# Kernel tuning notes

Measured on AMD Instinct MI355X. Metric: run time of the kernel, lower is better.

Reference implementation:

```python
import jax, jax.numpy as jnp
import numpy as np

B = 2097152
CXR, ECG, EHR = 15, 14, 13
TOTAL = CXR + ECG + EHR  # 42
LN_EPS = 1e-5


def setup_inputs() -> dict:
    key = jax.random.key(0)
    ks = jax.random.split(key, 40)
    f32 = jnp.float32
    inp = {
        "cxr_probs": jax.random.normal(ks[0], (B, CXR), dtype=f32),
        "ecg_probs": jax.random.normal(ks[1], (B, ECG), dtype=f32),
        "ehr_probs": jax.random.normal(ks[2], (B, EHR), dtype=f32),
    }
    for i, (name, E) in enumerate([("cxr", CXR), ("ecg", ECG), ("ehr", EHR)]):
        k0 = 3 + i * 8
        s_in = 1.0 / np.sqrt(E)
        s_kv = 1.0 / np.sqrt(TOTAL)
        inp[f"in_w_{name}"] = jax.random.normal(ks[k0], (3 * E, E), dtype=f32) * s_in
        inp[f"in_b_{name}"] = jnp.zeros((3 * E,), dtype=f32)
        inp[f"out_w_{name}"] = jax.random.normal(ks[k0 + 1], (E, E), dtype=f32) * s_in
        inp[f"out_b_{name}"] = jnp.zeros((E,), dtype=f32)
        inp[f"kv_w_{name}"] = jax.random.normal(ks[k0 + 2], (E, TOTAL), dtype=f32) * s_kv
        inp[f"kv_b_{name}"] = jax.random.normal(ks[k0 + 3], (E,), dtype=f32) * s_kv
        inp[f"ln_g_{name}"] = jnp.ones((E,), dtype=f32)
        inp[f"ln_b_{name}"] = jnp.zeros((E,), dtype=f32)
    return inp


def _branch(x, ctx, in_w, in_b, out_w, out_b, kv_w, kv_b, ln_g, ln_b):
    # x: [B, E], ctx: [B, 42]
    E = x.shape[-1]
    kv = ctx @ kv_w.T + kv_b                      # [B, E]
    # nn.MultiheadAttention with q_len = kv_len = 1: softmax over a single
    # key is identically 1, so attn_out == v_proj(kv) exactly.
    Wv, bv = in_w[2 * E:], in_b[2 * E:]
    v = kv @ Wv.T + bv                            # [B, E]
    attended = v @ out_w.T + out_b                # [B, E]
    y = x + attended
    mu = jnp.mean(y, axis=-1, keepdims=True)
    var = jnp.mean(jnp.square(y - mu), axis=-1, keepdims=True)
    return (y - mu) * jax.lax.rsqrt(var + LN_EPS) * ln_g + ln_b


def reference(cxr_probs, ecg_probs, ehr_probs,
              in_w_cxr, in_b_cxr, out_w_cxr, out_b_cxr, kv_w_cxr, kv_b_cxr, ln_g_cxr, ln_b_cxr,
              in_w_ecg, in_b_ecg, out_w_ecg, out_b_ecg, kv_w_ecg, kv_b_ecg, ln_g_ecg, ln_b_ecg,
              in_w_ehr, in_b_ehr, out_w_ehr, out_b_ehr, kv_w_ehr, kv_b_ehr, ln_g_ehr, ln_b_ehr):
    ctx = jnp.concatenate([cxr_probs, ecg_probs, ehr_probs], axis=1)  # [B, 42]
    cxr_out = _branch(cxr_probs, ctx, in_w_cxr, in_b_cxr, out_w_cxr, out_b_cxr,
                      kv_w_cxr, kv_b_cxr, ln_g_cxr, ln_b_cxr)
    ecg_out = _branch(ecg_probs, ctx, in_w_ecg, in_b_ecg, out_w_ecg, out_b_ecg,
                      kv_w_ecg, kv_b_ecg, ln_g_ecg, ln_b_ecg)
    ehr_out = _branch(ehr_probs, ctx, in_w_ehr, in_b_ehr, out_w_ehr, out_b_ehr,
                      kv_w_ehr, kv_b_ehr, ln_g_ehr, ln_b_ehr)
    return (cxr_out, ecg_out, ehr_out)
```

## Files before the change

kernel.cpp:

```cpp
#include <hip/hip_runtime.h>
#include <stdint.h>

constexpr int CXR = 15, ECG = 14, EHR = 13;
constexpr int TOTAL = 42;
constexpr int MPITCH = 44;
constexpr float LN_EPS = 1e-5f;

constexpr int WS_M    = 0;
constexpr int WS_B    = TOTAL * MPITCH;
constexpr int WS_G    = WS_B + TOTAL;
constexpr int WS_BETA = WS_G + TOTAL;
constexpr int WS_FRAG = 1976;

constexpr int WROWS = 64;
constexpr int S0F = 0, S1F = WROWS * CXR, S2F = S1F + WROWS * ECG;
constexpr int SEG_F   = S2F + WROWS * EHR;
constexpr int ARENA_F = SEG_F + 8;
constexpr int WC0 = WROWS * CXR / 4, WC1 = WROWS * ECG / 4, WC2 = WROWS * EHR / 4;

typedef _Float16 half8 __attribute__((ext_vector_type(8)));
typedef float float4v __attribute__((ext_vector_type(4)));

struct FuseArgs {
    const float *in_w, *in_b, *out_w, *out_b, *kv_w, *kv_b, *ln_g, *ln_b;
    int E, R;
};

__global__ void fuse_weights_kernel(FuseArgs a0, FuseArgs a1, FuseArgs a2,
                                    float* __restrict__ ws) {
    FuseArgs a = (blockIdx.x == 0) ? a0 : (blockIdx.x == 1 ? a1 : a2);
    const int E = a.E, R = a.R;
    const int tid = threadIdx.x;

    __shared__ float T1[15 * 42];
    __shared__ float b1[15];

    for (int idx = tid; idx < E * TOTAL; idx += blockDim.x) {
        int i = idx / TOTAL, j = idx % TOTAL;
        float acc = 0.f;
        for (int k = 0; k < E; ++k)
            acc = fmaf(a.in_w[(2 * E + i) * E + k], a.kv_w[k * TOTAL + j], acc);
        T1[i * TOTAL + j] = acc;
    }
    if (tid < E) {
        float acc = a.in_b[2 * E + tid];
        for (int k = 0; k < E; ++k)
            acc = fmaf(a.in_w[(2 * E + tid) * E + k], a.kv_b[k], acc);
        b1[tid] = acc;
    }
    __syncthreads();

    for (int idx = tid; idx < E * MPITCH; idx += blockDim.x) {
        int i = idx / MPITCH, j = idx % MPITCH;
        float acc = 0.f;
        if (j < TOTAL)
            for (int k = 0; k < E; ++k)
                acc = fmaf(a.out_w[i * E + k], T1[k * TOTAL + j], acc);
        ws[WS_M + (R + i) * MPITCH + j] = acc;
    }
    if (tid < E) {
        float acc = a.out_b[tid];
        for (int k = 0; k < E; ++k)
            acc = fmaf(a.out_w[tid * E + k], b1[k], acc);
        ws[WS_B + R + tid]    = acc;
        ws[WS_G + R + tid]    = a.ln_g[tid];
        ws[WS_BETA + R + tid] = a.ln_b[tid];
    }
}

__global__ void fuse_frags_kernel(float* __restrict__ ws) {
    const int tid = threadIdx.x;
    if (tid >= 384) return;
    const int l = tid & 63, nt = tid >> 6;
    const int m = nt >> 1, t = nt & 1;
    const int j = l & 15;
    const int k0 = t * 32 + 8 * (l >> 4);
    const int offm = (m == 0) ? 0 : (m == 1 ? CXR : CXR + ECG);
    const int Em   = (m == 0) ? CXR : (m == 1 ? ECG : EHR);
    half8 h;
#pragma unroll
    for (int i = 0; i < 8; ++i) {
        int pos = k0 + i;
        int g = -1;
        if (pos < 15) g = pos;
        else if (pos >= 16 && pos < 30) g = pos - 1;
        else if (pos >= 32 && pos < 45) g = pos - 3;
        float v = 0.f;
        if (j < Em && g >= 0) {
            int gr = offm + j;
            v = ws[WS_M + gr * MPITCH + g];
            if (g == gr) v += 1.f;
        }
        h[i] = (_Float16)v;
    }
    ((half8*)(ws + WS_FRAG))[nt * 64 + l] = h;
}

template <int CH>
__device__ __forceinline__ void stage_seg(const float* __restrict__ g,
                                          float* lds_seg_base, int lane) {
#pragma unroll
    for (int it = 0; it < (CH + 63) / 64; ++it) {
        int idx = lane + it * 64;
        if (idx < CH) {
            const __attribute__((address_space(1))) void* src =
                (const __attribute__((address_space(1))) void*)
                    ((const char*)g + (size_t)idx * 16);
            __attribute__((address_space(3))) void* dst =
                (__attribute__((address_space(3))) void*)
                    ((char*)lds_seg_base + it * 1024);
            __builtin_amdgcn_global_load_lds(src, dst, 16, 0, 0);
        }
    }
}

__global__ __launch_bounds__(128, 4) void cmca_main(
        const float* __restrict__ cxr, const float* __restrict__ ecg,
        const float* __restrict__ ehr, const float* __restrict__ ws,
        float* __restrict__ out_cxr, float* __restrict__ out_ecg,
        float* __restrict__ out_ehr) {
    __shared__ __align__(16) float sbuf[2 * ARENA_F];
    const int tid = threadIdx.x;
    const int w = tid >> 6, lane = tid & 63;
    float* stg = sbuf + w * ARENA_F;
    const size_t gw = (size_t)blockIdx.x * 2 + w;
    const int h = lane >> 4, b15 = lane & 15;

    stage_seg<WC0>(cxr + gw * (size_t)(WROWS * CXR), stg + S0F, lane);
    stage_seg<WC1>(ecg + gw * (size_t)(WROWS * ECG), stg + S1F, lane);
    stage_seg<WC2>(ehr + gw * (size_t)(WROWS * EHR), stg + S2F, lane);

    const half8* fr = (const half8*)(ws + WS_FRAG);
    half8 wf[3][2];
#pragma unroll
    for (int m = 0; m < 3; ++m)
#pragma unroll
        for (int t = 0; t < 2; ++t) wf[m][t] = fr[(m * 2 + t) * 64 + lane];

    asm volatile("s_waitcnt vmcnt(0)" ::: "memory");
    __builtin_amdgcn_sched_barrier(0);

    const int e0    = (h < 2) ? 15 : 14;
    const int base0 = ((h < 2) ? S0F : S1F) + (h & 1) * 8;
    const int off1  = (h == 1) ? 8 : 0;

    float4v acc[3][4];
#pragma unroll
    for (int m = 0; m < 3; ++m)
#pragma unroll
        for (int n = 0; n < 4; ++n) acc[m][n] = float4v{0.f, 0.f, 0.f, 0.f};

#pragma unroll
    for (int n = 0; n < 4; ++n) {
        const int batch = n * 16 + b15;
        const float* p0 = stg + base0 + batch * e0;
        const float* p1 = stg + S2F + off1 + batch * 13;
        half8 x0, x1;
#pragma unroll
        for (int e = 0; e < 8; ++e) x0[e] = (_Float16)p0[e];
#pragma unroll
        for (int e = 0; e < 8; ++e) x1[e] = (_Float16)p1[e];
#pragma unroll
        for (int m = 0; m < 3; ++m) {
            acc[m][n] = __builtin_amdgcn_mfma_f32_16x16x32_f16(
                wf[m][0], x0, acc[m][n], 0, 0, 0);
            acc[m][n] = __builtin_amdgcn_mfma_f32_16x16x32_f16(
                wf[m][1], x1, acc[m][n], 0, 0, 0);
        }
    }

    constexpr int Earr[3] = {CXR, ECG, EHR};
    constexpr int OFFa[3] = {0, CXR, CXR + ECG};
    constexpr int SEGF[3] = {S0F, S1F, S2F};
#pragma unroll
    for (int m = 0; m < 3; ++m) {
        const int E = Earr[m];
        const float invE = 1.0f / E;
        float bs[4], gm[4], bt[4];
#pragma unroll
        for (int r = 0; r < 4; ++r) {
            int j = 4 * h + r;
            bool v = j < E;
            bs[r] = v ? ws[WS_B + OFFa[m] + j] : 0.f;
            gm[r] = v ? ws[WS_G + OFFa[m] + j] : 0.f;
            bt[r] = v ? ws[WS_BETA + OFFa[m] + j] : 0.f;
        }
#pragma unroll
        for (int n = 0; n < 4; ++n) {
            float y0 = acc[m][n][0] + bs[0];
            float y1 = acc[m][n][1] + bs[1];
            float y2 = acc[m][n][2] + bs[2];
            float y3 = acc[m][n][3] + bs[3];
            float s  = (y0 + y1) + (y2 + y3);
            float ss = y0 * y0;
            ss = fmaf(y1, y1, ss);
            ss = fmaf(y2, y2, ss);
            ss = fmaf(y3, y3, ss);
            s  += __shfl_xor(s, 16, 64);
            ss += __shfl_xor(ss, 16, 64);
            s  += __shfl_xor(s, 32, 64);
            ss += __shfl_xor(ss, 32, 64);
            float mu  = s * invE;
            float var = fmaf(ss, invE, -mu * mu);
            float rs  = rsqrtf(var + LN_EPS);
            const int row = n * 16 + b15;
            float yv[4] = {y0, y1, y2, y3};
#pragma unroll
            for (int r = 0; r < 4; ++r) {
                int j = 4 * h + r;
                if (j < E)
                    stg[SEGF[m] + row * E + j] =
                        fmaf((yv[r] - mu) * rs, gm[r], bt[r]);
            }
        }
    }

    const float4v* w4 = (const float4v*)stg;
    float4v* o0 = (float4v*)(out_cxr + gw * (size_t)(WROWS * CXR));
    float4v* o1 = (float4v*)(out_ecg + gw * (size_t)(WROWS * ECG));
    float4v* o2 = (float4v*)(out_ehr + gw * (size_t)(WROWS * EHR));
#pragma unroll
    for (int it = 0; it < 4; ++it) {
        int idx = lane + it * 64;
        if (idx < WC0) o0[idx] = w4[idx];
    }
#pragma unroll
    for (int it = 0; it < 4; ++it) {
        int idx = lane + it * 64;
        if (idx < WC1) o1[idx] = w4[WC0 + idx];
    }
#pragma unroll
    for (int it = 0; it < 4; ++it) {
        int idx = lane + it * 64;
        if (idx < WC2) o2[idx] = w4[WC0 + WC1 + idx];
    }
}

extern "C" void kernel_launch(void* const* d_in, const int* in_sizes, int n_in,
                              void* d_out, int out_size, void* d_ws, size_t ws_size,
                              hipStream_t stream) {
    const float* cxr = (const float*)d_in[0];
    const float* ecg = (const float*)d_in[1];
    const float* ehr = (const float*)d_in[2];
    float* ws = (float*)d_ws;
    float* out = (float*)d_out;

    const size_t Bn = (size_t)in_sizes[0] / CXR;

    auto mk = [&](int base, int E, int R) {
        FuseArgs a;
        a.in_w  = (const float*)d_in[base + 0];
        a.in_b  = (const float*)d_in[base + 1];
        a.out_w = (const float*)d_in[base + 2];
        a.out_b = (const float*)d_in[base + 3];
        a.kv_w  = (const float*)d_in[base + 4];
        a.kv_b  = (const float*)d_in[base + 5];
        a.ln_g  = (const float*)d_in[base + 6];
        a.ln_b  = (const float*)d_in[base + 7];
        a.E = E; a.R = R;
        return a;
    };
    FuseArgs a0 = mk(3, CXR, 0);
    FuseArgs a1 = mk(11, ECG, CXR);
    FuseArgs a2 = mk(19, EHR, CXR + ECG);

    fuse_weights_kernel<<<3, 256, 0, stream>>>(a0, a1, a2, ws);
    fuse_frags_kernel<<<1, 384, 0, stream>>>(ws);

    const int nblocks = (int)(Bn / (WROWS * 2));
    cmca_main<<<nblocks, 128, 0, stream>>>(cxr, ecg, ehr, ws,
                                           out,
                                           out + Bn * CXR,
                                           out + Bn * (CXR + ECG));
}
```

Baseline: 152.2 us.

## Repack staged inputs into swizzled fp16 rows with bias folded into GEMM

```diff
diff --git a/kernel.cpp b/kernel.cpp
--- a/kernel.cpp
+++ b/kernel.cpp
@@ -14,11 +14,11 @@
 
 constexpr int WROWS = 64;
 constexpr int S0F = 0, S1F = WROWS * CXR, S2F = S1F + WROWS * ECG;
-constexpr int SEG_F   = S2F + WROWS * EHR;
-constexpr int ARENA_F = SEG_F + 8;
 constexpr int WC0 = WROWS * CXR / 4, WC1 = WROWS * ECG / 4, WC2 = WROWS * EHR / 4;
+constexpr int ARENA_B = 11264;
 
 typedef _Float16 half8 __attribute__((ext_vector_type(8)));
+typedef __fp16 fp16x2 __attribute__((ext_vector_type(2)));
 typedef float float4v __attribute__((ext_vector_type(4)));
 
 struct FuseArgs {
@@ -80,16 +80,16 @@
     half8 h;
 #pragma unroll
     for (int i = 0; i < 8; ++i) {
-        int pos = k0 + i;
-        int g = -1;
-        if (pos < 15) g = pos;
-        else if (pos >= 16 && pos < 30) g = pos - 1;
-        else if (pos >= 32 && pos < 45) g = pos - 3;
+        int k = k0 + i;
         float v = 0.f;
-        if (j < Em && g >= 0) {
-            int gr = offm + j;
-            v = ws[WS_M + gr * MPITCH + g];
-            if (g == gr) v += 1.f;
+        if (j < Em) {
+            int glob = offm + j;
+            if (k < TOTAL) {
+                v = ws[WS_M + glob * MPITCH + k];
+                if (k == glob) v += 1.f;
+            } else if (k == TOTAL) {
+                v = ws[WS_B + glob];
+            }
         }
         h[i] = (_Float16)v;
     }
@@ -114,21 +114,22 @@
     }
 }
 
-__global__ __launch_bounds__(128, 4) void cmca_main(
+__global__ __launch_bounds__(128) void cmca_main(
         const float* __restrict__ cxr, const float* __restrict__ ecg,
         const float* __restrict__ ehr, const float* __restrict__ ws,
         float* __restrict__ out_cxr, float* __restrict__ out_ecg,
         float* __restrict__ out_ehr) {
-    __shared__ __align__(16) float sbuf[2 * ARENA_F];
+    __shared__ __align__(16) char smem[2 * ARENA_B];
     const int tid = threadIdx.x;
     const int w = tid >> 6, lane = tid & 63;
-    float* stg = sbuf + w * ARENA_F;
+    char* arena = smem + w * ARENA_B;
+    float* af = (float*)arena;
     const size_t gw = (size_t)blockIdx.x * 2 + w;
     const int h = lane >> 4, b15 = lane & 15;
 
-    stage_seg<WC0>(cxr + gw * (size_t)(WROWS * CXR), stg + S0F, lane);
-    stage_seg<WC1>(ecg + gw * (size_t)(WROWS * ECG), stg + S1F, lane);
-    stage_seg<WC2>(ehr + gw * (size_t)(WROWS * EHR), stg + S2F, lane);
+    stage_seg<WC0>(cxr + gw * (size_t)(WROWS * CXR), af + S0F, lane);
+    stage_seg<WC1>(ecg + gw * (size_t)(WROWS * ECG), af + S1F, lane);
+    stage_seg<WC2>(ehr + gw * (size_t)(WROWS * EHR), af + S2F, lane);
 
     const half8* fr = (const half8*)(ws + WS_FRAG);
     half8 wf[3][2];
@@ -140,34 +141,66 @@
     asm volatile("s_waitcnt vmcnt(0)" ::: "memory");
     __builtin_amdgcn_sched_barrier(0);
 
-    const int e0    = (h < 2) ? 15 : 14;
-    const int base0 = ((h < 2) ? S0F : S1F) + (h & 1) * 8;
-    const int off1  = (h == 1) ? 8 : 0;
+    float x[TOTAL];
+#pragma unroll
+    for (int j = 0; j < CXR; ++j) x[j] = af[S0F + lane * CXR + j];
+#pragma unroll
+    for (int j = 0; j < ECG; ++j) x[CXR + j] = af[S1F + lane * ECG + j];
+#pragma unroll
+    for (int j = 0; j < EHR; ++j) x[CXR + ECG + j] = af[S2F + lane * EHR + j];
+    asm volatile("s_waitcnt lgkmcnt(0)" ::: "memory");
+    __builtin_amdgcn_sched_barrier(0);
+
+    const int swz = (lane & 7) << 4;
+    {
+#pragma unroll
+        for (int j = 0; j < 5; ++j) {
+            union { fp16x2 p[4]; half8 v; } u;
+#pragma unroll
+            for (int q = 0; q < 4; ++q)
+                u.p[q] = __builtin_amdgcn_cvt_pkrtz(x[j * 8 + 2 * q],
+                                                    x[j * 8 + 2 * q + 1]);
+            *(half8*)(arena + ((lane * 128 + j * 16) ^ swz)) = u.v;
+        }
+        union { fp16x2 p[4]; half8 v; } u;
+        u.p[0] = __builtin_amdgcn_cvt_pkrtz(x[40], x[41]);
+        u.p[1] = __builtin_amdgcn_cvt_pkrtz(1.f, 0.f);
+        u.p[2] = __builtin_amdgcn_cvt_pkrtz(0.f, 0.f);
+        u.p[3] = u.p[2];
+        *(half8*)(arena + ((lane * 128 + 80) ^ swz)) = u.v;
+        float4v z = float4v{0.f, 0.f, 0.f, 0.f};
+        *(float4v*)(arena + ((lane * 128 + 96) ^ swz))  = z;
+        *(float4v*)(arena + ((lane * 128 + 112) ^ swz)) = z;
+    }
+    __builtin_amdgcn_sched_barrier(0);
+
+    half8 xf[4][2];
+#pragma unroll
+    for (int n = 0; n < 4; ++n) {
+        int row = n * 16 + b15;
+        int rsw = (row & 7) << 4;
+#pragma unroll
+        for (int t2 = 0; t2 < 2; ++t2)
+            xf[n][t2] = *(const half8*)(arena +
+                ((row * 128 + t2 * 64 + h * 16) ^ rsw));
+    }
+    asm volatile("s_waitcnt lgkmcnt(0)" ::: "memory");
+    __builtin_amdgcn_sched_barrier(0);
 
     float4v acc[3][4];
 #pragma unroll
     for (int m = 0; m < 3; ++m)
 #pragma unroll
         for (int n = 0; n < 4; ++n) acc[m][n] = float4v{0.f, 0.f, 0.f, 0.f};
-
-#pragma unroll
-    for (int n = 0; n < 4; ++n) {
-        const int batch = n * 16 + b15;
-        const float* p0 = stg + base0 + batch * e0;
-        const float* p1 = stg + S2F + off1 + batch * 13;
-        half8 x0, x1;
-#pragma unroll
-        for (int e = 0; e < 8; ++e) x0[e] = (_Float16)p0[e];
-#pragma unroll
-        for (int e = 0; e < 8; ++e) x1[e] = (_Float16)p1[e];
-#pragma unroll
-        for (int m = 0; m < 3; ++m) {
-            acc[m][n] = __builtin_amdgcn_mfma_f32_16x16x32_f16(
-                wf[m][0], x0, acc[m][n], 0, 0, 0);
-            acc[m][n] = __builtin_amdgcn_mfma_f32_16x16x32_f16(
-                wf[m][1], x1, acc[m][n], 0, 0, 0);
-        }
-    }
+#pragma unroll
+    for (int t2 = 0; t2 < 2; ++t2)
+#pragma unroll
+        for (int m = 0; m < 3; ++m)
+#pragma unroll
+            for (int n = 0; n < 4; ++n)
+                acc[m][n] = __builtin_amdgcn_mfma_f32_16x16x32_f16(
+                    wf[m][t2], xf[n][t2], acc[m][n], 0, 0, 0);
+    __builtin_amdgcn_sched_barrier(0);
 
     constexpr int Earr[3] = {CXR, ECG, EHR};
     constexpr int OFFa[3] = {0, CXR, CXR + ECG};
@@ -176,21 +209,18 @@
     for (int m = 0; m < 3; ++m) {
         const int E = Earr[m];
         const float invE = 1.0f / E;
-        float bs[4], gm[4], bt[4];
+        float gm[4], bt[4];
 #pragma unroll
         for (int r = 0; r < 4; ++r) {
             int j = 4 * h + r;
             bool v = j < E;
-            bs[r] = v ? ws[WS_B + OFFa[m] + j] : 0.f;
             gm[r] = v ? ws[WS_G + OFFa[m] + j] : 0.f;
             bt[r] = v ? ws[WS_BETA + OFFa[m] + j] : 0.f;
         }
 #pragma unroll
         for (int n = 0; n < 4; ++n) {
-            float y0 = acc[m][n][0] + bs[0];
-            float y1 = acc[m][n][1] + bs[1];
-            float y2 = acc[m][n][2] + bs[2];
-            float y3 = acc[m][n][3] + bs[3];
+            float y0 = acc[m][n][0], y1 = acc[m][n][1];
+            float y2 = acc[m][n][2], y3 = acc[m][n][3];
             float s  = (y0 + y1) + (y2 + y3);
             float ss = y0 * y0;
             ss = fmaf(y1, y1, ss);
@@ -209,13 +239,14 @@
             for (int r = 0; r < 4; ++r) {
                 int j = 4 * h + r;
                 if (j < E)
-                    stg[SEGF[m] + row * E + j] =
+                    af[SEGF[m] + row * E + j] =
                         fmaf((yv[r] - mu) * rs, gm[r], bt[r]);
             }
         }
     }
-
-    const float4v* w4 = (const float4v*)stg;
+    __builtin_amdgcn_sched_barrier(0);
+
+    const float4v* w4 = (const float4v*)af;
     float4v* o0 = (float4v*)(out_cxr + gw * (size_t)(WROWS * CXR));
     float4v* o1 = (float4v*)(out_ecg + gw * (size_t)(WROWS * ECG));
     float4v* o2 = (float4v*)(out_ehr + gw * (size_t)(WROWS * EHR));
```

After: 152.8 us. About the same (+0.4%).
